# Kernel tuning notes

Measured on AMD Instinct MI355X. Metric: run time of the kernel, lower is better.

The kernel has to match this reference:

```python
import jax, jax.numpy as jnp
import numpy as np


def setup_inputs() -> dict:
    key = jax.random.key(0)
    k1, k2, k3 = jax.random.split(key, 3)
    bs, S, d, C = 2, 196, 512, 1006
    imgFeaturemap = jax.random.normal(k1, (bs, S, d), dtype=jnp.float32)
    wordFeatures = jax.random.normal(k2, (C, d), dtype=jnp.float32)
    fc3_w = jax.random.normal(k3, (d, d), dtype=jnp.float32) * 0.02
    fc3_b = jnp.zeros((d,), dtype=jnp.float32)
    return {"imgFeaturemap": imgFeaturemap, "wordFeatures": wordFeatures,
            "fc3_w": fc3_w, "fc3_b": fc3_b}


def reference(imgFeaturemap, wordFeatures, fc3_w, fc3_b):
    # imgFeaturemap: (bs, S, d); wordFeatures: (C, d)
    # Broadcast multiply + tanh: (bs, S, C, d)
    t = jnp.tanh(imgFeaturemap[:, :, None, :] * wordFeatures[None, None, :, :])
    # Per-row Linear (PyTorch Linear: x @ W^T + b)
    feat = jnp.einsum('bscd,ed->bsce', t, fc3_w) + fc3_b
    # Softmax over spatial axis S (axis=1), independently per (class, channel)
    coef = jax.nn.softmax(feat, axis=1)
    # Softmax-weighted spatial pooling per class: (bs, C, d)
    semanticFeature = jnp.einsum('bsd,bscd->bcd', imgFeaturemap, coef)
    return semanticFeature
```

## Files before the change

kernel.cpp:

```cpp
#include <hip/hip_runtime.h>

using half8   = __attribute__((ext_vector_type(8))) _Float16;
using floatx4 = __attribute__((ext_vector_type(4))) float;

namespace {
constexpr int S = 196, D = 512, C = 1006;
constexpr int CB   = 16;
constexpr int EBLK = 256;
constexpr int BK   = 64;
constexpr int TPB  = 512;
constexpr int RS   = 64;
constexpr float KTANH = 2.885390082f;
constexpr float INVK  = 0.34657359028f;
constexpr float LOG2E = 1.44269504f;


__device__ __forceinline__ int sw_off(int row, int seg) {
    return row * RS + ((seg ^ (row & 7)) << 3);
}

__device__ __forceinline__ void gload16(const _Float16* g, _Float16* l) {
    __builtin_amdgcn_global_load_lds(
        (const __attribute__((address_space(1))) unsigned int*)g,
        (__attribute__((address_space(3))) unsigned int*)l, 16, 0, 0);
}

__device__ __forceinline__ _Float16 tanh_ps(float y) {
    float e = __builtin_amdgcn_exp2f(y);
    return (_Float16)(1.0f - 2.0f * __builtin_amdgcn_rcpf(e + 1.0f));
}

__device__ __forceinline__ half8 tanh8(floatx4 i0, floatx4 i1, floatx4 w0, floatx4 w1) {
    half8 t;
    t[0] = tanh_ps(i0[0] * w0[0]); t[1] = tanh_ps(i0[1] * w0[1]);
    t[2] = tanh_ps(i0[2] * w0[2]); t[3] = tanh_ps(i0[3] * w0[3]);
    t[4] = tanh_ps(i1[0] * w1[0]); t[5] = tanh_ps(i1[1] * w1[1]);
    t[6] = tanh_ps(i1[2] * w1[2]); t[7] = tanh_ps(i1[3] * w1[3]);
    return t;
}

__global__ void prep_w16sw(const float* __restrict__ fw, _Float16* __restrict__ W16sw) {
    int id = blockIdx.x * blockDim.x + threadIdx.x;
    int kki = id >> 12;
    int r   = (id >> 3) & 511;
    int j   = id & 7;
    const float* src = fw + (size_t)r * D + kki * BK + j * 8;
    floatx4 v0 = *(const floatx4*)src;
    floatx4 v1 = *(const floatx4*)(src + 4);
    half8 h;
    h[0] = (_Float16)(v0[0] * LOG2E); h[1] = (_Float16)(v0[1] * LOG2E);
    h[2] = (_Float16)(v0[2] * LOG2E); h[3] = (_Float16)(v0[3] * LOG2E);
    h[4] = (_Float16)(v1[0] * LOG2E); h[5] = (_Float16)(v1[1] * LOG2E);
    h[6] = (_Float16)(v1[2] * LOG2E); h[7] = (_Float16)(v1[3] * LOG2E);
    *(half8*)&W16sw[((size_t)kki << 15) + r * RS + ((j ^ (r & 7)) << 3)] = h;
}

__global__ __launch_bounds__(TPB, 2) void semdec_mfma(
    const float* __restrict__ img, const float* __restrict__ word,
    const _Float16* __restrict__ W16sw, float* __restrict__ out)
{
    __shared__ __align__(16) _Float16 Wc[2][EBLK * RS];
    __shared__ __align__(16) _Float16 Tc[2][8 * CB * RS];
    __shared__ __align__(16) float imgS[8][D];

    const int ct = blockIdx.x;
    const int b  = blockIdx.y;
    const int et = blockIdx.z;

    const int tid  = threadIdx.x;
    const int lane = tid & 63;
    const int wv   = tid >> 6;
    const int l15  = lane & 15;
    const int quad = lane >> 4;
    const int sg   = wv >> 2;
    const int ew   = wv & 3;

    const int c0 = ct * CB;
    const int e0 = et * EBLK;

    const int sT2  = tid >> 7;
    const int ciT  = (tid >> 3) & 15;
    const int segT = tid & 7;
    int cgT = c0 + ciT; if (cgT > C - 1) cgT = C - 1;
    const float* wordRowT = word + (size_t)cgT * D + segT * 8;

    floatx4 lacc[4], aacc[4];
    #pragma unroll
    for (int ej = 0; ej < 4; ++ej) {
        lacc[ej] = (floatx4){0.f, 0.f, 0.f, 0.f};
        aacc[ej] = (floatx4){0.f, 0.f, 0.f, 0.f};
    }

    const float* imgB = img + (size_t)b * S * D;
    constexpr int NPASS = 25;

    floatx4 wc0 = *(const floatx4*)(wordRowT);
    floatx4 wc1 = *(const floatx4*)(wordRowT + 4);
    floatx4 wn0 = *(const floatx4*)(wordRowT + BK);
    floatx4 wn1 = *(const floatx4*)(wordRowT + BK + 4);

    {
        const _Float16* wg = W16sw + ((size_t)e0 << 6);
        #pragma unroll
        for (int it = 0; it < 4; ++it) {
            int o = ((wv * 4 + it) << 9) + (lane << 3);
            gload16(wg + o, &Wc[0][o]);
        }
    }

    for (int pr = 0; pr < NPASS; ++pr) {
        const int s0 = pr * 8;
        const int slim = (pr == NPASS - 1) ? 4 : 8;

        __syncthreads();
        #pragma unroll
        for (int it = 0; it < 2; ++it) {
            int idx = it * TPB + tid;
            int row = idx >> 7, pos = (idx & 127) << 2;
            int srow = s0 + row; if (srow > S - 1) srow = S - 1;
            floatx4 v = *(const floatx4*)&imgB[(size_t)srow * D + pos];
            floatx4 sv = {v[0] * KTANH, v[1] * KTANH, v[2] * KTANH, v[3] * KTANH};
            *(floatx4*)&imgS[row][pos] = sv;
        }
        __syncthreads();

        #pragma unroll
        for (int it = 0; it < 2; ++it) {
            int sl = it * 4 + sT2;
            const float* ip = &imgS[sl][segT * 8];
            floatx4 i0 = *(const floatx4*)ip;
            floatx4 i1 = *(const floatx4*)(ip + 4);
            *(half8*)&Tc[0][sw_off(sl * CB + ciT, segT)] = tanh8(i0, i1, wc0, wc1);
        }
        wc0 = wn0; wc1 = wn1;

        floatx4 acc[4][4];
        #pragma unroll
        for (int si = 0; si < 4; ++si)
            #pragma unroll
            for (int ej = 0; ej < 4; ++ej)
                acc[si][ej] = (floatx4){0.f, 0.f, 0.f, 0.f};

        for (int kk = 0; kk < 8; ++kk) {
            const int p = kk & 1;
            __syncthreads();

            {
                const _Float16* wg = W16sw + ((size_t)((kk + 1) & 7) << 15) + ((size_t)e0 << 6);
                #pragma unroll
                for (int it = 0; it < 4; ++it) {
                    int o = ((wv * 4 + it) << 9) + (lane << 3);
                    gload16(wg + o, &Wc[p ^ 1][o]);
                }
            }

            {
                const int kc = ((kk + 2) & 7) * BK;
                wn0 = *(const floatx4*)(wordRowT + kc);
                wn1 = *(const floatx4*)(wordRowT + kc + 4);
            }

            {
                half8 bf[4], af[4];
                #pragma unroll
                for (int ej = 0; ej < 4; ++ej)
                    bf[ej] = *(const half8*)&Wc[p][sw_off(ew * 64 + ej * 16 + l15, quad)];
                #pragma unroll
                for (int si = 0; si < 4; ++si)
                    af[si] = *(const half8*)&Tc[p][sw_off((sg * 4 + si) * CB + l15, quad)];
                #pragma unroll
                for (int si = 0; si < 4; ++si)
                    #pragma unroll
                    for (int ej = 0; ej < 4; ++ej)
                        acc[si][ej] = __builtin_amdgcn_mfma_f32_16x16x32_f16(
                            af[si], bf[ej], acc[si][ej], 0, 0, 0);
            }

            if (kk < 7) {
                #pragma unroll
                for (int it = 0; it < 2; ++it) {
                    int sl = it * 4 + sT2;
                    const float* ip = &imgS[sl][((kk + 1) << 6) + segT * 8];
                    floatx4 i0 = *(const floatx4*)ip;
                    floatx4 i1 = *(const floatx4*)(ip + 4);
                    *(half8*)&Tc[p ^ 1][sw_off(sl * CB + ciT, segT)] = tanh8(i0, i1, wc0, wc1);
                }
                wc0 = wn0; wc1 = wn1;
            }

            {
                half8 bf[4], af[4];
                #pragma unroll
                for (int ej = 0; ej < 4; ++ej)
                    bf[ej] = *(const half8*)&Wc[p][sw_off(ew * 64 + ej * 16 + l15, 4 + quad)];
                #pragma unroll
                for (int si = 0; si < 4; ++si)
                    af[si] = *(const half8*)&Tc[p][sw_off((sg * 4 + si) * CB + l15, 4 + quad)];
                #pragma unroll
                for (int si = 0; si < 4; ++si)
                    #pragma unroll
                    for (int ej = 0; ej < 4; ++ej)
                        acc[si][ej] = __builtin_amdgcn_mfma_f32_16x16x32_f16(
                            af[si], bf[ej], acc[si][ej], 0, 0, 0);
            }
        }

        #pragma unroll
        for (int si = 0; si < 4; ++si) {
            const int sl = sg * 4 + si;
            if (sl >= slim) break;
            #pragma unroll
            for (int ej = 0; ej < 4; ++ej) {
                float ie = imgS[sl][e0 + ew * 64 + ej * 16 + l15] * INVK;
                #pragma unroll
                for (int r = 0; r < 4; ++r) {
                    float ev = __builtin_amdgcn_exp2f(acc[si][ej][r]);
                    lacc[ej][r] += ev;
                    aacc[ej][r] += ie * ev;
                }
            }
        }
    }

    __syncthreads();
    float* red = (float*)&Wc[0][0];
    if (sg == 1) {
        const int base = (tid - 256) * 32;
        #pragma unroll
        for (int ej = 0; ej < 4; ++ej)
            #pragma unroll
            for (int r = 0; r < 4; ++r) {
                red[base + ej * 8 + r * 2]     = lacc[ej][r];
                red[base + ej * 8 + r * 2 + 1] = aacc[ej][r];
            }
    }
    __syncthreads();
    if (sg == 0) {
        const int base = tid * 32;
        #pragma unroll
        for (int r = 0; r < 4; ++r) {
            const int cg = c0 + quad * 4 + r;
            if (cg < C) {
                #pragma unroll
                for (int ej = 0; ej < 4; ++ej) {
                    float l = lacc[ej][r] + red[base + ej * 8 + r * 2];
                    float a = aacc[ej][r] + red[base + ej * 8 + r * 2 + 1];
                    const int eg = e0 + ew * 64 + ej * 16 + l15;
                    out[((size_t)b * C + cg) * D + eg] = a / l;
                }
            }
        }
    }
}

}

extern "C" void kernel_launch(void* const* d_in, const int* in_sizes, int n_in,
                              void* d_out, int out_size, void* d_ws, size_t ws_size,
                              hipStream_t stream) {
    const float* img  = (const float*)d_in[0];
    const float* word = (const float*)d_in[1];
    const float* fw   = (const float*)d_in[2];
    float* out = (float*)d_out;

    _Float16* W16sw = (_Float16*)d_ws;

    hipLaunchKernelGGL(prep_w16sw, dim3(128), dim3(256), 0, stream, fw, W16sw);
    hipLaunchKernelGGL(semdec_mfma, dim3(64, 2, 2), dim3(TPB), 0, stream,
                       img, word, W16sw, out);
}
```

Baseline: 326.7 us.

## Load fc3 weight fragments directly from global into registers instead of LDS staging

The weight tile is no longer staged into double-buffered LDS via global_load_lds. Each lane now reads its MFMA B-operand fragments straight from a row-major fp16 copy of the weight, relying on L1/L2 caching. This frees a large LDS allocation, which may allow higher occupancy, and removes the LDS write/read traffic for weights. The cost is exposed global-load latency inside the k-loop without explicit prefetch. The reduction buffer becomes a dedicated padded array with stride 33 to avoid bank conflicts.

```diff
diff --git a/kernel.cpp b/kernel.cpp
--- a/kernel.cpp
+++ b/kernel.cpp
@@ -19,12 +19,6 @@
     return row * RS + ((seg ^ (row & 7)) << 3);
 }
 
-__device__ __forceinline__ void gload16(const _Float16* g, _Float16* l) {
-    __builtin_amdgcn_global_load_lds(
-        (const __attribute__((address_space(1))) unsigned int*)g,
-        (__attribute__((address_space(3))) unsigned int*)l, 16, 0, 0);
-}
-
 __device__ __forceinline__ _Float16 tanh_ps(float y) {
     float e = __builtin_amdgcn_exp2f(y);
     return (_Float16)(1.0f - 2.0f * __builtin_amdgcn_rcpf(e + 1.0f));
@@ -39,12 +33,11 @@
     return t;
 }
 
-__global__ void prep_w16sw(const float* __restrict__ fw, _Float16* __restrict__ W16sw) {
+__global__ void prep_w16(const float* __restrict__ fw, _Float16* __restrict__ W16) {
     int id = blockIdx.x * blockDim.x + threadIdx.x;
-    int kki = id >> 12;
-    int r   = (id >> 3) & 511;
-    int j   = id & 7;
-    const float* src = fw + (size_t)r * D + kki * BK + j * 8;
+    int r  = id >> 6;
+    int j  = id & 63;
+    const float* src = fw + (size_t)r * D + j * 8;
     floatx4 v0 = *(const floatx4*)src;
     floatx4 v1 = *(const floatx4*)(src + 4);
     half8 h;
@@ -52,16 +45,16 @@
     h[2] = (_Float16)(v0[2] * LOG2E); h[3] = (_Float16)(v0[3] * LOG2E);
     h[4] = (_Float16)(v1[0] * LOG2E); h[5] = (_Float16)(v1[1] * LOG2E);
     h[6] = (_Float16)(v1[2] * LOG2E); h[7] = (_Float16)(v1[3] * LOG2E);
-    *(half8*)&W16sw[((size_t)kki << 15) + r * RS + ((j ^ (r & 7)) << 3)] = h;
+    *(half8*)&W16[(size_t)r * D + j * 8] = h;
 }
 
 __global__ __launch_bounds__(TPB, 2) void semdec_mfma(
     const float* __restrict__ img, const float* __restrict__ word,
-    const _Float16* __restrict__ W16sw, float* __restrict__ out)
+    const _Float16* __restrict__ W16, float* __restrict__ out)
 {
-    __shared__ __align__(16) _Float16 Wc[2][EBLK * RS];
     __shared__ __align__(16) _Float16 Tc[2][8 * CB * RS];
     __shared__ __align__(16) float imgS[8][D];
+    __shared__ __align__(16) float red[256 * 33];
 
     const int ct = blockIdx.x;
     const int b  = blockIdx.y;
@@ -78,6 +71,8 @@
     const int c0 = ct * CB;
     const int e0 = et * EBLK;
 
+    const _Float16* wbase = W16 + (size_t)(e0 + ew * 64 + l15) * D + quad * 8;
+
     const int sT2  = tid >> 7;
     const int ciT  = (tid >> 3) & 15;
     const int segT = tid & 7;
@@ -98,15 +93,6 @@
     floatx4 wc1 = *(const floatx4*)(wordRowT + 4);
     floatx4 wn0 = *(const floatx4*)(wordRowT + BK);
     floatx4 wn1 = *(const floatx4*)(wordRowT + BK + 4);
-
-    {
-        const _Float16* wg = W16sw + ((size_t)e0 << 6);
-        #pragma unroll
-        for (int it = 0; it < 4; ++it) {
-            int o = ((wv * 4 + it) << 9) + (lane << 3);
-            gload16(wg + o, &Wc[0][o]);
-        }
-    }
 
     for (int pr = 0; pr < NPASS; ++pr) {
         const int s0 = pr * 8;
@@ -145,14 +131,10 @@
             const int p = kk & 1;
             __syncthreads();
 
-            {
-                const _Float16* wg = W16sw + ((size_t)((kk + 1) & 7) << 15) + ((size_t)e0 << 6);
-                #pragma unroll
-                for (int it = 0; it < 4; ++it) {
-                    int o = ((wv * 4 + it) << 9) + (lane << 3);
-                    gload16(wg + o, &Wc[p ^ 1][o]);
-                }
-            }
+            half8 bf0[4];
+            #pragma unroll
+            for (int ej = 0; ej < 4; ++ej)
+                bf0[ej] = *(const half8*)(wbase + (size_t)ej * 16 * D + kk * BK);
 
             {
                 const int kc = ((kk + 2) & 7) * BK;
@@ -161,10 +143,7 @@
             }
 
             {
-                half8 bf[4], af[4];
-                #pragma unroll
-                for (int ej = 0; ej < 4; ++ej)
-                    bf[ej] = *(const half8*)&Wc[p][sw_off(ew * 64 + ej * 16 + l15, quad)];
+                half8 af[4];
                 #pragma unroll
                 for (int si = 0; si < 4; ++si)
                     af[si] = *(const half8*)&Tc[p][sw_off((sg * 4 + si) * CB + l15, quad)];
@@ -173,8 +152,13 @@
                     #pragma unroll
                     for (int ej = 0; ej < 4; ++ej)
                         acc[si][ej] = __builtin_amdgcn_mfma_f32_16x16x32_f16(
-                            af[si], bf[ej], acc[si][ej], 0, 0, 0);
-            }
+                            af[si], bf0[ej], acc[si][ej], 0, 0, 0);
+            }
+
+            half8 bf1[4];
+            #pragma unroll
+            for (int ej = 0; ej < 4; ++ej)
+                bf1[ej] = *(const half8*)(wbase + (size_t)ej * 16 * D + kk * BK + 32);
 
             if (kk < 7) {
                 #pragma unroll
@@ -189,10 +173,7 @@
             }
 
             {
-                half8 bf[4], af[4];
-                #pragma unroll
-                for (int ej = 0; ej < 4; ++ej)
-                    bf[ej] = *(const half8*)&Wc[p][sw_off(ew * 64 + ej * 16 + l15, 4 + quad)];
+                half8 af[4];
                 #pragma unroll
                 for (int si = 0; si < 4; ++si)
                     af[si] = *(const half8*)&Tc[p][sw_off((sg * 4 + si) * CB + l15, 4 + quad)];
@@ -201,7 +182,7 @@
                     #pragma unroll
                     for (int ej = 0; ej < 4; ++ej)
                         acc[si][ej] = __builtin_amdgcn_mfma_f32_16x16x32_f16(
-                            af[si], bf[ej], acc[si][ej], 0, 0, 0);
+                            af[si], bf1[ej], acc[si][ej], 0, 0, 0);
             }
         }
 
@@ -223,9 +204,8 @@
     }
 
     __syncthreads();
-    float* red = (float*)&Wc[0][0];
     if (sg == 1) {
-        const int base = (tid - 256) * 32;
+        const int base = (tid - 256) * 33;
         #pragma unroll
         for (int ej = 0; ej < 4; ++ej)
             #pragma unroll
@@ -236,7 +216,7 @@
     }
     __syncthreads();
     if (sg == 0) {
-        const int base = tid * 32;
+        const int base = tid * 33;
         #pragma unroll
         for (int r = 0; r < 4; ++r) {
             const int cg = c0 + quad * 4 + r;
@@ -263,9 +243,9 @@
     const float* fw   = (const float*)d_in[2];
     float* out = (float*)d_out;
 
-    _Float16* W16sw = (_Float16*)d_ws;
-
-    hipLaunchKernelGGL(prep_w16sw, dim3(128), dim3(256), 0, stream, fw, W16sw);
+    _Float16* W16 = (_Float16*)d_ws;
+
+    hipLaunchKernelGGL(prep_w16, dim3(128), dim3(256), 0, stream, fw, W16);
     hipLaunchKernelGGL(semdec_mfma, dim3(64, 2, 2), dim3(TPB), 0, stream,
-                       img, word, W16sw, out);
-}
+                       img, word, W16, out);
+}
```

Measured after the change: 474.8 us. 45.3% more time.
